# Optimization experiments

Measured on AMD Instinct MI355X. Metric: run time of the kernel, lower is better.

## Reference

```python
import jax, jax.numpy as jnp
import numpy as np

L, H, E, D, FF, V, CTX = 8, 16, 1024, 64, 4096, 2048, 2048
B, T = 4, 1024


def _ln(x, g, b, eps=1e-5):
    mu = x.mean(-1, keepdims=True)
    var = ((x - mu) ** 2).mean(-1, keepdims=True)
    return (x - mu) * jax.lax.rsqrt(var + eps) * g + b


def setup_inputs() -> dict:
    key = jax.random.key(0)
    ks = jax.random.split(key, 12)
    s = 0.02
    return {
        "tokens": jax.random.randint(ks[0], (B, T), 0, V),
        "tok_emb": jax.random.normal(ks[1], (V, E), jnp.float32) * s,
        "pos_emb": jax.random.normal(ks[2], (CTX, E), jnp.float32) * s,
        "Wq": jax.random.normal(ks[3], (L, H, E, D), jnp.float32) * s,
        "Wk": jax.random.normal(ks[4], (L, H, E, D), jnp.float32) * s,
        "Wv": jax.random.normal(ks[5], (L, H, E, D), jnp.float32) * s,
        "Wo": jax.random.normal(ks[6], (L, H * D, E), jnp.float32) * s,
        "bo": jnp.zeros((L, E), jnp.float32),
        "ln1_g": jnp.ones((L, E), jnp.float32),
        "ln1_b": jnp.zeros((L, E), jnp.float32),
        "ln2_g": jnp.ones((L, E), jnp.float32),
        "ln2_b": jnp.zeros((L, E), jnp.float32),
        "W1": jax.random.normal(ks[7], (L, E, FF), jnp.float32) * s,
        "b1": jnp.zeros((L, FF), jnp.float32),
        "W2": jax.random.normal(ks[8], (L, FF, E), jnp.float32) * s,
        "b2": jnp.zeros((L, E), jnp.float32),
        "lnf_g": jnp.ones((E,), jnp.float32),
        "lnf_b": jnp.zeros((E,), jnp.float32),
        "Wlm": jax.random.normal(ks[9], (E, V), jnp.float32) * s,
        "blm": jnp.zeros((V,), jnp.float32),
    }


def reference(tokens, tok_emb, pos_emb, Wq, Wk, Wv, Wo, bo, ln1_g, ln1_b,
              ln2_g, ln2_b, W1, b1, W2, b2, lnf_g, lnf_b, Wlm, blm):
    # NOTE: original indexes pos_embd with token ids (pos_embd(x.int()))
    x = tok_emb[tokens] + pos_emb[tokens]  # [B,T,E]
    t = x.shape[1]
    causal = jnp.tril(jnp.ones((t, t), bool))
    scale = 1.0 / jnp.sqrt(jnp.float32(D))
    for l in range(L):
        x = _ln(x, ln1_g[l], ln1_b[l])
        q = jnp.einsum('bte,hed->bhtd', x, Wq[l])
        k = jnp.einsum('bte,hed->bhtd', x, Wk[l])
        v = jnp.einsum('bte,hed->bhtd', x, Wv[l])
        scores = jnp.einsum('bhtd,bhsd->bhts', q, k) * scale
        scores = jnp.where(causal, scores, -jnp.inf)
        att = jax.nn.softmax(scores, axis=-1)
        o = jnp.einsum('bhts,bhsd->bhtd', att, v)
        o = o.transpose(0, 2, 1, 3).reshape(x.shape[0], t, H * D)
        x = x + o @ Wo[l] + bo[l]
        x = _ln(x, ln2_g[l], ln2_b[l])
        x = x + jax.nn.relu(x @ W1[l] + b1[l]) @ W2[l] + b2[l]
    x = _ln(x, lnf_g, lnf_b)
    return x @ Wlm + blm
```

## Files before the change

kernel.cpp:

```cpp
#include <hip/hip_runtime.h>
#include <hip/hip_bf16.h>

#define LAYERS 8
#define H_ 16
#define E_ 1024
#define D_ 64
#define FF_ 4096
#define V_ 2048
#define B_ 4
#define T_ 1024
#define MTOK (B_*T_)

typedef __bf16 bf16x8_t __attribute__((ext_vector_type(8)));
typedef __bf16 bf16x4_t __attribute__((ext_vector_type(4)));
typedef float f32x4_t __attribute__((ext_vector_type(4)));
typedef __hip_bfloat16 bf16_t;

__device__ __forceinline__ bf16_t f2b(float f) { return __float2bfloat16(f); }

__global__ void embed_kernel(const int* __restrict__ tokens,
                             const float* __restrict__ te,
                             const float* __restrict__ pe,
                             bf16_t* __restrict__ x) {
  int row = blockIdx.x;
  int tok = tokens[row];
  int t = threadIdx.x;
  float4 va = ((const float4*)(te + (size_t)tok * E_))[t];
  float4 vp = ((const float4*)(pe + (size_t)tok * E_))[t];
  bf16x4_t o;
  o[0] = (__bf16)(va.x + vp.x); o[1] = (__bf16)(va.y + vp.y);
  o[2] = (__bf16)(va.z + vp.z); o[3] = (__bf16)(va.w + vp.w);
  ((bf16x4_t*)(x + (size_t)row * E_))[t] = o;
}

__global__ __launch_bounds__(256) void ln_kernel(const bf16_t* __restrict__ xin,
                                                 bf16_t* __restrict__ xout,
                                                 const float* __restrict__ g,
                                                 const float* __restrict__ b) {
  int row = blockIdx.x, tid = threadIdx.x;
  bf16x4_t v4 = ((const bf16x4_t*)(xin + (size_t)row * E_))[tid];
  float v0 = (float)v4[0], v1 = (float)v4[1], v2 = (float)v4[2], v3 = (float)v4[3];
  float s  = v0 + v1 + v2 + v3;
  float sq = v0*v0 + v1*v1 + v2*v2 + v3*v3;
  for (int off = 32; off; off >>= 1) {
    s  += __shfl_xor(s, off, 64);
    sq += __shfl_xor(sq, off, 64);
  }
  __shared__ float2 wred[4];
  if ((tid & 63) == 0) wred[tid >> 6] = make_float2(s, sq);
  __syncthreads();
  float2 w0 = wred[0], w1 = wred[1], w2 = wred[2], w3 = wred[3];
  float S = w0.x + w1.x + w2.x + w3.x, SQ = w0.y + w1.y + w2.y + w3.y;
  float mean = S * (1.0f / E_);
  float var  = SQ * (1.0f / E_) - mean * mean;
  float inv = rsqrtf(var + 1e-5f);
  float4 gv = ((const float4*)g)[tid];
  float4 bv = ((const float4*)b)[tid];
  bf16x4_t o;
  o[0] = (__bf16)((v0 - mean) * inv * gv.x + bv.x);
  o[1] = (__bf16)((v1 - mean) * inv * gv.y + bv.y);
  o[2] = (__bf16)((v2 - mean) * inv * gv.z + bv.z);
  o[3] = (__bf16)((v3 - mean) * inv * gv.w + bv.w);
  ((bf16x4_t*)(xout + (size_t)row * E_))[tid] = o;
}

__global__ __launch_bounds__(256) void reduce_ln_kernel(
    const bf16_t* __restrict__ p,
    const bf16_t* __restrict__ tin,
    const float* __restrict__ bias,
    bf16_t* __restrict__ r,
    bf16_t* __restrict__ tout,
    const float* __restrict__ g,
    const float* __restrict__ b) {
  int row = blockIdx.x, tid = threadIdx.x;
  size_t base = (size_t)row * E_ + tid * 4;
  bf16x4_t tv = *(const bf16x4_t*)(tin + base);
  bf16x4_t p0 = *(const bf16x4_t*)(p + base);
  bf16x4_t p1 = *(const bf16x4_t*)(p + (size_t)MTOK * E_ + base);
  float4 bv = ((const float4*)bias)[tid];
  float y0 = (float)tv[0] + (float)p0[0] + (float)p1[0] + bv.x;
  float y1 = (float)tv[1] + (float)p0[1] + (float)p1[1] + bv.y;
  float y2 = (float)tv[2] + (float)p0[2] + (float)p1[2] + bv.z;
  float y3 = (float)tv[3] + (float)p0[3] + (float)p1[3] + bv.w;
  bf16x4_t rv;
  rv[0] = (__bf16)y0; rv[1] = (__bf16)y1; rv[2] = (__bf16)y2; rv[3] = (__bf16)y3;
  *(bf16x4_t*)(r + base) = rv;
  float z0 = (float)rv[0], z1 = (float)rv[1], z2 = (float)rv[2], z3 = (float)rv[3];
  float s = z0 + z1 + z2 + z3, sq = z0*z0 + z1*z1 + z2*z2 + z3*z3;
  for (int off = 32; off; off >>= 1) {
    s  += __shfl_xor(s, off, 64);
    sq += __shfl_xor(sq, off, 64);
  }
  __shared__ float2 wred[4];
  if ((tid & 63) == 0) wred[tid >> 6] = make_float2(s, sq);
  __syncthreads();
  float2 w0 = wred[0], w1 = wred[1], w2 = wred[2], w3 = wred[3];
  float S = w0.x + w1.x + w2.x + w3.x, SQ = w0.y + w1.y + w2.y + w3.y;
  float mean = S * (1.0f / E_);
  float var  = SQ * (1.0f / E_) - mean * mean;
  float inv = rsqrtf(var + 1e-5f);
  float4 gv = ((const float4*)g)[tid];
  float4 b2v = ((const float4*)b)[tid];
  bf16x4_t o;
  o[0] = (__bf16)((z0 - mean) * inv * gv.x + b2v.x);
  o[1] = (__bf16)((z1 - mean) * inv * gv.y + b2v.y);
  o[2] = (__bf16)((z2 - mean) * inv * gv.z + b2v.z);
  o[3] = (__bf16)((z3 - mean) * inv * gv.w + b2v.w);
  *(bf16x4_t*)(tout + base) = o;
}

__global__ void prep_weights_kernel(const float* __restrict__ Wq,
                                    const float* __restrict__ Wk,
                                    const float* __restrict__ Wv,
                                    const float* __restrict__ Wo,
                                    const float* __restrict__ W1,
                                    const float* __restrict__ W2,
                                    bf16_t* __restrict__ WqkvT,
                                    bf16_t* __restrict__ WoT,
                                    bf16_t* __restrict__ W1T,
                                    bf16_t* __restrict__ W2T,
                                    int l) {
  __shared__ float tile[32][33];
  int bid = blockIdx.x;
  const float* src; bf16_t* dst; int R, C, r0, c0;
  if (bid < 3072) {
    int op = bid >> 10, rem = bid & 1023;
    int h = rem >> 6, tt = rem & 63;
    const float* W = (op == 0) ? Wq : (op == 1) ? Wk : Wv;
    src = W + (size_t)l * H_ * E_ * D_ + (size_t)h * E_ * D_;
    dst = WqkvT + (size_t)op * E_ * H_ * D_ + (size_t)h * E_ * D_;
    R = E_; C = D_; r0 = (tt >> 1) * 32; c0 = (tt & 1) * 32;
  } else if (bid < 4096) {
    int tt = bid - 3072;
    src = Wo + (size_t)l * H_ * D_ * E_; dst = WoT;
    R = H_ * D_; C = E_; r0 = (tt >> 5) * 32; c0 = (tt & 31) * 32;
  } else if (bid < 8192) {
    int tt = bid - 4096;
    src = W1 + (size_t)l * E_ * FF_; dst = W1T;
    R = E_; C = FF_; r0 = (tt >> 7) * 32; c0 = (tt & 127) * 32;
  } else {
    int tt = bid - 8192;
    src = W2 + (size_t)l * FF_ * E_; dst = W2T;
    R = FF_; C = E_; r0 = (tt >> 5) * 32; c0 = (tt & 31) * 32;
  }
  int tx = threadIdx.x, ty = threadIdx.y;
  for (int i = 0; i < 4; i++)
    tile[ty + i * 8][tx] = src[(size_t)(r0 + ty + i * 8) * C + (c0 + tx)];
  __syncthreads();
  for (int i = 0; i < 4; i++)
    dst[(size_t)(c0 + ty + i * 8) * R + (r0 + tx)] = f2b(tile[tx][ty + i * 8]);
}

__global__ void transpose_kernel(const float* __restrict__ in, bf16_t* __restrict__ out,
                                 int R, int C) {
  __shared__ float tile[32][33];
  int r0 = blockIdx.y * 32, c0 = blockIdx.x * 32;
  int tx = threadIdx.x, ty = threadIdx.y;
  for (int i = 0; i < 4; i++)
    tile[ty + i * 8][tx] = in[(size_t)(r0 + ty + i * 8) * C + (c0 + tx)];
  __syncthreads();
  for (int i = 0; i < 4; i++)
    out[(size_t)(c0 + ty + i * 8) * R + (r0 + tx)] = f2b(tile[tx][ty + i * 8]);
}

enum { MODE_F32 = 0, MODE_BF16 = 1, MODE_QKV = 2, MODE_BF16R = 3 };

__device__ __forceinline__ void gload16(const bf16_t* g, bf16_t* l) {
  __builtin_amdgcn_global_load_lds((const __attribute__((address_space(1))) void*)g,
                                   (__attribute__((address_space(3))) void*)l, 16, 0, 0);
}

__device__ __forceinline__ int xcd_swz(int flat, int nwg) {
  int q = nwg >> 3, r = nwg & 7;
  int xcd = flat & 7, idx = flat >> 3;
  return (xcd < r ? xcd * (q + 1) : r * (q + 1) + (xcd - r) * q) + idx;
}

#define BK 32
template <int BM, int BN, int MODE>
__global__ __launch_bounds__(256) void gemm97_kernel(
    const bf16_t* __restrict__ A, long long sAz, int lda,
    const bf16_t* __restrict__ Bt, long long sBz, int ldb,
    void* __restrict__ C, long long sCz,
    const float* __restrict__ bias,
    const void* __restrict__ resid,
    int M, int N, int K, int relu) {
  constexpr int FR = BM / 32, FC = BN / 32;
  constexpr int A_ISS = BM / 64, B_ISS = BN / 64;
  __shared__ __align__(16) bf16_t As[2][BM * BK];
  __shared__ __align__(16) bf16_t Bs[2][BN * BK];
  int tid = threadIdx.x;
  int z = blockIdx.z;
  int nwg = gridDim.x * gridDim.y;
  int flat = xcd_swz(blockIdx.y * gridDim.x + blockIdx.x, nwg);
  int m0 = (flat / gridDim.x) * BM, n0 = (flat % gridDim.x) * BN;
  const bf16_t* Ab = A + (size_t)z * sAz + (size_t)m0 * lda;
  const bf16_t* Bb = Bt + (size_t)z * sBz + (size_t)n0 * ldb;
  int lane = tid & 63, wave = tid >> 6;
  int wr = (wave >> 1) * (BM / 2), wc = (wave & 1) * (BN / 2);
  int lr = lane & 15, lk = (lane >> 4) * 8;
  int srow = tid >> 2;
  int scol = (tid & 3) * 8;

  f32x4_t acc[FR][FC];
  for (int i = 0; i < FR; i++)
    for (int j = 0; j < FC; j++)
      acc[i][j] = (f32x4_t){0.f, 0.f, 0.f, 0.f};

  auto stage = [&](int buf, int k0) {
#pragma unroll
    for (int i = 0; i < A_ISS; i++)
      gload16(Ab + (size_t)(i * 64 + srow) * lda + k0 + scol, &As[buf][i * 2048 + wave * 512]);
#pragma unroll
    for (int i = 0; i < B_ISS; i++)
      gload16(Bb + (size_t)(i * 64 + srow) * ldb + k0 + scol, &Bs[buf][i * 2048 + wave * 512]);
  };

  int nk = K / BK;
  stage(0, 0);
  __syncthreads();
  int cur = 0;
  for (int kt = 0; kt < nk; ++kt) {
    if (kt + 1 < nk) stage(cur ^ 1, (kt + 1) * BK);
    bf16x8_t af[FR], bfv[FC];
#pragma unroll
    for (int i = 0; i < FR; i++)
      af[i] = *(const bf16x8_t*)(&As[cur][(wr + i * 16 + lr) * BK + lk]);
#pragma unroll
    for (int j = 0; j < FC; j++)
      bfv[j] = *(const bf16x8_t*)(&Bs[cur][(wc + j * 16 + lr) * BK + lk]);
#pragma unroll
    for (int i = 0; i < FR; i++)
#pragma unroll
      for (int j = 0; j < FC; j++)
        acc[i][j] = __builtin_amdgcn_mfma_f32_16x16x32_bf16(af[i], bfv[j], acc[i][j], 0, 0, 0);
    __syncthreads();
    cur ^= 1;
  }

#pragma unroll
  for (int i = 0; i < FR; i++)
#pragma unroll
    for (int j = 0; j < FC; j++) {
      f32x4_t v = acc[i][j];
      int n = n0 + wc + j * 16 + lr;
      int mb = m0 + wr + i * 16 + (lane >> 4) * 4;
#pragma unroll
      for (int r = 0; r < 4; r++) {
        int m = mb + r;
        float val = v[r];
        if (bias) val += bias[n];
        if (relu) val = fmaxf(val, 0.f);
        if (MODE == MODE_F32) {
          size_t idx = (size_t)z * sCz + (size_t)m * N + n;
          ((float*)C)[idx] = val;
        } else if (MODE == MODE_BF16) {
          size_t idx = (size_t)z * sCz + (size_t)m * N + n;
          ((bf16_t*)C)[idx] = f2b(val);
        } else if (MODE == MODE_BF16R) {
          size_t idx = (size_t)m * N + n;
          val += __bfloat162float(((const bf16_t*)resid)[idx]);
          ((bf16_t*)C)[idx] = f2b(val);
        } else {
          int sect = n >> 10, hd = n & 1023, h = hd >> 6, d = hd & 63;
          int b = m >> 10, t = m & 1023;
          size_t base = (size_t)sect * ((size_t)B_ * H_ * T_ * D_);
          size_t idx = base + ((size_t)(b * H_ + h) << 16) +
                       (sect == 2 ? (size_t)((d << 10) + t) : (size_t)((t << 6) + d));
          ((bf16_t*)C)[idx] = f2b(val);
        }
      }
    }
}

template <int MODE>
__global__ __launch_bounds__(512) void gemm3_kernel(
    const bf16_t* __restrict__ A, int lda,
    const bf16_t* __restrict__ Bt, int ldb,
    void* __restrict__ C, long long sCz,
    const float* __restrict__ bias,
    int M, int N, int kspan, int relu) {
  constexpr int ABUFE = 256 * 64;
  constexpr int BBUFE = 128 * 64;
  __shared__ __align__(16) bf16_t LA[3 * ABUFE];
  __shared__ __align__(16) bf16_t LB[3 * BBUFE];
  int tid = threadIdx.x, lane = tid & 63, wave = tid >> 6;
  int wm = wave >> 1, wn = wave & 1;
  int z = blockIdx.z;
  int nwg = gridDim.x * gridDim.y;
  int flat = xcd_swz(blockIdx.y * gridDim.x + blockIdx.x, nwg);
  int m0 = (flat / gridDim.x) * 256, n0 = (flat % gridDim.x) * 128;
  const bf16_t* Ab = A + (size_t)m0 * lda + (size_t)z * kspan;
  const bf16_t* Bb = Bt + (size_t)n0 * ldb + (size_t)z * kspan;
  int sr = lane & 15, sc = (lane >> 4) * 8;

  f32x4_t acc[4][4];
#pragma unroll
  for (int i = 0; i < 4; i++)
#pragma unroll
    for (int j = 0; j < 4; j++)
      acc[i][j] = (f32x4_t){0.f, 0.f, 0.f, 0.f};

  auto stageh = [&](int b, int kt, int h) {
    int kg = kt * 64;
#pragma unroll
    for (int ch = 0; ch < 2; ch++) {
      int sub = wave * 4 + 2 * h + ch;
      gload16(Ab + (size_t)((sub >> 1) * 16 + sr) * lda + kg + (sub & 1) * 32 + sc,
              LA + b * ABUFE + sub * 512);
    }
    {
      int sub = wave * 2 + h;
      gload16(Bb + (size_t)((sub >> 1) * 16 + sr) * ldb + kg + (sub & 1) * 32 + sc,
              LB + b * BBUFE + sub * 512);
    }
  };

  auto phase = [&](int b, int ks, int t, int nk) {
    bf16x8_t af[4], bfv[4];
    unsigned abase = (unsigned)(size_t)(LA + b * ABUFE);
    unsigned bbase = (unsigned)(size_t)(LB + b * BBUFE);
#pragma unroll
    for (int i = 0; i < 4; i++) {
      unsigned ad = abase + (unsigned)((((wm * 4 + i) * 2 + ks) * 512 + lane * 8) * 2);
      asm volatile("ds_read_b128 %0, %1" : "=v"(af[i]) : "v"(ad));
    }
#pragma unroll
    for (int j = 0; j < 4; j++) {
      unsigned bd = bbase + (unsigned)((((wn * 4 + j) * 2 + ks) * 512 + lane * 8) * 2);
      asm volatile("ds_read_b128 %0, %1" : "=v"(bfv[j]) : "v"(bd));
    }
    if (t + 2 < nk) stageh((t + 2) % 3, t + 2, ks);
    __builtin_amdgcn_s_barrier();
    asm volatile("s_waitcnt lgkmcnt(0)" ::: "memory");
    __builtin_amdgcn_sched_barrier(0);
    __builtin_amdgcn_s_setprio(1);
#pragma unroll
    for (int i = 0; i < 4; i++)
#pragma unroll
      for (int j = 0; j < 4; j++)
        acc[i][j] = __builtin_amdgcn_mfma_f32_16x16x32_bf16(af[i], bfv[j], acc[i][j], 0, 0, 0);
    __builtin_amdgcn_s_setprio(0);
  };

  int nk = kspan / 64;
  stageh(0, 0, 0); stageh(0, 0, 1);
  stageh(1, 1, 0); stageh(1, 1, 1);
  for (int t = 0; t < nk; ++t) {
    int b = t % 3;
    if (t + 1 < nk) { asm volatile("s_waitcnt vmcnt(6)" ::: "memory"); }
    else            { asm volatile("s_waitcnt vmcnt(0)" ::: "memory"); }
    __builtin_amdgcn_s_barrier();
    phase(b, 0, t, nk);
    phase(b, 1, t, nk);
  }

#pragma unroll
  for (int i = 0; i < 4; i++)
#pragma unroll
    for (int j = 0; j < 4; j++) {
      f32x4_t v = acc[i][j];
      int n = n0 + wn * 64 + j * 16 + (lane & 15);
      int mb = m0 + wm * 64 + i * 16 + (lane >> 4) * 4;
#pragma unroll
      for (int r = 0; r < 4; r++) {
        int m = mb + r;
        float val = v[r];
        if (bias) val += bias[n];
        if (relu) val = fmaxf(val, 0.f);
        if (MODE == MODE_F32) {
          size_t idx = (size_t)z * sCz + (size_t)m * N + n;
          ((float*)C)[idx] = val;
        } else {
          size_t idx = (size_t)z * sCz + (size_t)m * N + n;
          ((bf16_t*)C)[idx] = f2b(val);
        }
      }
    }
}

#define KPAD 72

__global__ __launch_bounds__(256) void flash_kernel(
    const bf16_t* __restrict__ q,
    const bf16_t* __restrict__ kk,
    const bf16_t* __restrict__ vt,
    bf16_t* __restrict__ o) {
  __shared__ __align__(16) bf16_t Ks[64 * KPAD];
  __shared__ __align__(16) bf16_t Vs[64 * KPAD];
  __shared__ __align__(16) bf16_t Ps[4][16 * KPAD];
  int bid = blockIdx.x;
  int qi = 15 - (bid >> 6);
  int bh = bid & 63;
  int b = bh >> 4, h = bh & 15;
  const bf16_t* qb = q + ((size_t)bh << 16);
  const bf16_t* kb = kk + ((size_t)bh << 16);
  const bf16_t* vb = vt + ((size_t)bh << 16);
  int tid = threadIdx.x, lane = tid & 63, wave = tid >> 6;
  int lr = lane & 15, lg = lane >> 4;
  int qbase = qi * 64;

  bf16x8_t qf[2];
  {
    const bf16_t* qrow = qb + (size_t)(qbase + wave * 16 + lr) * D_ + lg * 8;
    qf[0] = *(const bf16x8_t*)(qrow);
    qf[1] = *(const bf16x8_t*)(qrow + 32);
  }

  float m_r[4], l_r[4];
  f32x4_t oc[4];
#pragma unroll
  for (int r = 0; r < 4; r++) { m_r[r] = -1e30f; l_r[r] = 0.f; }
#pragma unroll
  for (int j = 0; j < 4; j++) oc[j] = (f32x4_t){0.f, 0.f, 0.f, 0.f};

  int srow = tid >> 2, scol = (tid & 3) * 16;

  bf16x8_t k0, k1, v0, v1;
  {
    const bf16_t* kg = kb + (size_t)srow * D_ + scol;
    k0 = *(const bf16x8_t*)kg;
    k1 = *(const bf16x8_t*)(kg + 8);
    const bf16_t* vg = vb + (size_t)srow * T_ + scol;
    v0 = *(const bf16x8_t*)vg;
    v1 = *(const bf16x8_t*)(vg + 8);
  }

  for (int s = 0; s <= qi; s++) {
    __syncthreads();
    *(bf16x8_t*)(&Ks[srow * KPAD + scol]) = k0;
    *(bf16x8_t*)(&Ks[srow * KPAD + scol + 8]) = k1;
    *(bf16x8_t*)(&Vs[srow * KPAD + scol]) = v0;
    *(bf16x8_t*)(&Vs[srow * KPAD + scol + 8]) = v1;
    __syncthreads();

    if (s < qi) {
      int kv1 = (s + 1) * 64;
      const bf16_t* kg = kb + (size_t)(kv1 + srow) * D_ + scol;
      k0 = *(const bf16x8_t*)kg;
      k1 = *(const bf16x8_t*)(kg + 8);
      const bf16_t* vg = vb + (size_t)srow * T_ + kv1 + scol;
      v0 = *(const bf16x8_t*)vg;
      v1 = *(const bf16x8_t*)(vg + 8);
    }

    int kv0 = s * 64;
    f32x4_t sc[4];
#pragma unroll
    for (int j = 0; j < 4; j++) {
      f32x4_t a = (f32x4_t){0.f, 0.f, 0.f, 0.f};
      bf16x8_t b0 = *(const bf16x8_t*)(&Ks[(j * 16 + lr) * KPAD + lg * 8]);
      bf16x8_t b1 = *(const bf16x8_t*)(&Ks[(j * 16 + lr) * KPAD + lg * 8 + 32]);
      a = __builtin_amdgcn_mfma_f32_16x16x32_bf16(qf[0], b0, a, 0, 0, 0);
      a = __builtin_amdgcn_mfma_f32_16x16x32_bf16(qf[1], b1, a, 0, 0, 0);
      sc[j] = a;
    }
    if (s == qi) {
#pragma unroll
      for (int j = 0; j < 4; j++)
#pragma unroll
        for (int r = 0; r < 4; r++) {
          int kvp = kv0 + j * 16 + lr;
          int qp  = qbase + wave * 16 + lg * 4 + r;
          sc[j][r] = (kvp <= qp) ? sc[j][r] * 0.125f : -1e30f;
        }
    } else {
#pragma unroll
      for (int j = 0; j < 4; j++)
#pragma unroll
        for (int r = 0; r < 4; r++) sc[j][r] *= 0.125f;
    }

    float pm[4];
#pragma unroll
    for (int r = 0; r < 4; r++) {
      float v = fmaxf(fmaxf(sc[0][r], sc[1][r]), fmaxf(sc[2][r], sc[3][r]));
      v = fmaxf(v, __shfl_xor(v, 1, 64));
      v = fmaxf(v, __shfl_xor(v, 2, 64));
      v = fmaxf(v, __shfl_xor(v, 4, 64));
      v = fmaxf(v, __shfl_xor(v, 8, 64));
      pm[r] = v;
    }
    bool ok = (pm[0] - m_r[0] <= 8.f) && (pm[1] - m_r[1] <= 8.f) &&
              (pm[2] - m_r[2] <= 8.f) && (pm[3] - m_r[3] <= 8.f);
    if (!__all(ok)) {
#pragma unroll
      for (int r = 0; r < 4; r++) {
        float mn = fmaxf(m_r[r], pm[r]);
        float ex = __expf(m_r[r] - mn);
        m_r[r] = mn;
        l_r[r] *= ex;
#pragma unroll
        for (int j = 0; j < 4; j++) oc[j][r] *= ex;
      }
    }
#pragma unroll
    for (int j = 0; j < 4; j++)
#pragma unroll
      for (int r = 0; r < 4; r++) {
        float p = __expf(sc[j][r] - m_r[r]);
        l_r[r] += p;
        Ps[wave][(lg * 4 + r) * KPAD + j * 16 + lr] = f2b(p);
      }

    bf16x8_t pa0 = *(const bf16x8_t*)(&Ps[wave][lr * KPAD + lg * 8]);
    bf16x8_t pa1 = *(const bf16x8_t*)(&Ps[wave][lr * KPAD + lg * 8 + 32]);
#pragma unroll
    for (int j = 0; j < 4; j++) {
      bf16x8_t vb0 = *(const bf16x8_t*)(&Vs[(j * 16 + lr) * KPAD + lg * 8]);
      bf16x8_t vb1 = *(const bf16x8_t*)(&Vs[(j * 16 + lr) * KPAD + lg * 8 + 32]);
      oc[j] = __builtin_amdgcn_mfma_f32_16x16x32_bf16(pa0, vb0, oc[j], 0, 0, 0);
      oc[j] = __builtin_amdgcn_mfma_f32_16x16x32_bf16(pa1, vb1, oc[j], 0, 0, 0);
    }
  }

#pragma unroll
  for (int r = 0; r < 4; r++) {
    float v = l_r[r];
    v += __shfl_xor(v, 1, 64);
    v += __shfl_xor(v, 2, 64);
    v += __shfl_xor(v, 4, 64);
    v += __shfl_xor(v, 8, 64);
    l_r[r] = 1.f / v;
  }
  bf16_t* ob = o + ((size_t)(b * T_ + qbase + wave * 16)) * (H_ * D_) + h * D_;
#pragma unroll
  for (int j = 0; j < 4; j++)
#pragma unroll
    for (int r = 0; r < 4; r++) {
      int qrow = lg * 4 + r;
      ob[(size_t)qrow * (H_ * D_) + j * 16 + lr] = f2b(oc[j][r] * l_r[r]);
    }
}

extern "C" void kernel_launch(void* const* d_in, const int* in_sizes, int n_in,
                              void* d_out, int out_size, void* d_ws, size_t ws_size,
                              hipStream_t stream) {
  (void)in_sizes; (void)n_in; (void)out_size; (void)ws_size;
  const int*   tokens = (const int*)d_in[0];
  const float* tok_emb = (const float*)d_in[1];
  const float* pos_emb = (const float*)d_in[2];
  const float* Wq = (const float*)d_in[3];
  const float* Wk = (const float*)d_in[4];
  const float* Wv = (const float*)d_in[5];
  const float* Wo = (const float*)d_in[6];
  const float* bo = (const float*)d_in[7];
  const float* ln1_g = (const float*)d_in[8];
  const float* ln1_b = (const float*)d_in[9];
  const float* ln2_g = (const float*)d_in[10];
  const float* ln2_b = (const float*)d_in[11];
  const float* W1 = (const float*)d_in[12];
  const float* b1 = (const float*)d_in[13];
  const float* W2 = (const float*)d_in[14];
  const float* b2 = (const float*)d_in[15];
  const float* lnf_g = (const float*)d_in[16];
  const float* lnf_b = (const float*)d_in[17];
  const float* Wlm = (const float*)d_in[18];
  const float* blm = (const float*)d_in[19];

  char* w = (char*)d_ws;
  size_t off = 0;
  auto alloc = [&](size_t bytes) { void* p = (void*)(w + off); off += (bytes + 255) & ~(size_t)255; return p; };
  bf16_t* r    = (bf16_t*)alloc((size_t)MTOK * E_ * 2);
  bf16_t* t    = (bf16_t*)alloc((size_t)MTOK * E_ * 2);
  bf16_t* q    = (bf16_t*)alloc((size_t)B_ * H_ * T_ * D_ * 2);
  bf16_t* kk   = (bf16_t*)alloc((size_t)B_ * H_ * T_ * D_ * 2);
  bf16_t* vt   = (bf16_t*)alloc((size_t)B_ * H_ * T_ * D_ * 2);
  bf16_t* o    = (bf16_t*)alloc((size_t)MTOK * E_ * 2);
  bf16_t* h1   = (bf16_t*)alloc((size_t)MTOK * FF_ * 2);
  bf16_t* WqkvT = (bf16_t*)alloc((size_t)3 * E_ * H_ * D_ * 2);
  bf16_t* WoT  = (bf16_t*)alloc((size_t)E_ * H_ * D_ * 2);
  bf16_t* W1T  = (bf16_t*)alloc((size_t)E_ * FF_ * 2);
  bf16_t* W2T  = (bf16_t*)alloc((size_t)E_ * FF_ * 2);
  bf16_t* WlmT = (bf16_t*)alloc((size_t)E_ * V_ * 2);
  bf16_t* p2   = (bf16_t*)alloc((size_t)2 * MTOK * E_ * 2);

  embed_kernel<<<MTOK, 256, 0, stream>>>(tokens, tok_emb, pos_emb, r);
  transpose_kernel<<<dim3(V_ / 32, E_ / 32), dim3(32, 8), 0, stream>>>(Wlm, WlmT, E_, V_);
  ln_kernel<<<MTOK, 256, 0, stream>>>(r, t, ln1_g, ln1_b);

  for (int l = 0; l < LAYERS; l++) {
    prep_weights_kernel<<<12288, dim3(32, 8), 0, stream>>>(
        Wq, Wk, Wv, Wo, W1, W2, WqkvT, WoT, W1T, W2T, l);

    gemm97_kernel<128, 128, MODE_QKV><<<dim3(24, 32, 1), 256, 0, stream>>>(
        t, 0, E_, WqkvT, 0, E_, q, 0, nullptr, nullptr, MTOK, 3 * H_ * D_, E_, 0);

    flash_kernel<<<1024, 256, 0, stream>>>(q, kk, vt, o);

    gemm97_kernel<128, 128, MODE_BF16R><<<dim3(8, 32, 1), 256, 0, stream>>>(
        o, 0, H_ * D_, WoT, 0, H_ * D_, r, 0, bo + l * E_, t, MTOK, E_, H_ * D_, 0);

    ln_kernel<<<MTOK, 256, 0, stream>>>(r, t, ln2_g + l * E_, ln2_b + l * E_);

    gemm3_kernel<MODE_BF16><<<dim3(32, 16, 1), 512, 0, stream>>>(
        t, E_, W1T, E_, h1, 0, b1 + l * FF_, MTOK, FF_, E_, 1);
    gemm3_kernel<MODE_BF16><<<dim3(8, 16, 2), 512, 0, stream>>>(
        h1, FF_, W2T, FF_, p2, (long long)MTOK * E_, nullptr, MTOK, E_, FF_ / 2, 0);
    const float* gn = (l + 1 < LAYERS) ? (ln1_g + (l + 1) * E_) : lnf_g;
    const float* bn = (l + 1 < LAYERS) ? (ln1_b + (l + 1) * E_) : lnf_b;
    reduce_ln_kernel<<<MTOK, 256, 0, stream>>>(p2, t, b2 + l * E_, r, t, gn, bn);
  }

  gemm3_kernel<MODE_F32><<<dim3(16, 16, 1), 512, 0, stream>>>(
      t, E_, WlmT, E_, d_out, 0, blm, MTOK, V_, E_, 0);
}
```

Baseline: 2.098 ms.

## Vectorize LN kernels to two rows per block, widen weight transpose tiles, add MFMA priority

The LayerNorm and residual+LayerNorm kernels now process two rows per 256-thread block, with 8-element bf16 vector loads and stores per thread. The per-layer weight prep transpose moves from 32x32 to 64x64 tiles, using float4 reads and 16-byte bf16 writes to cut launch count and raise memory-transaction width. The flash attention kernel wraps its MFMA blocks in s_setprio to favour matrix issue over other waves. The changes aim to reduce memory-bound overhead in the small kernels; the transpose now does strided LDS column reads that may cause bank conflicts.

```diff
diff --git a/kernel.cpp b/kernel.cpp
--- a/kernel.cpp
+++ b/kernel.cpp
@@ -37,11 +37,15 @@
                                                  bf16_t* __restrict__ xout,
                                                  const float* __restrict__ g,
                                                  const float* __restrict__ b) {
-  int row = blockIdx.x, tid = threadIdx.x;
-  bf16x4_t v4 = ((const bf16x4_t*)(xin + (size_t)row * E_))[tid];
-  float v0 = (float)v4[0], v1 = (float)v4[1], v2 = (float)v4[2], v3 = (float)v4[3];
-  float s  = v0 + v1 + v2 + v3;
-  float sq = v0*v0 + v1*v1 + v2*v2 + v3*v3;
+  int tid = threadIdx.x;
+  int row = blockIdx.x * 2 + (tid >> 7);
+  int li = tid & 127;
+  size_t base = (size_t)row * E_ + li * 8;
+  bf16x8_t v8 = *(const bf16x8_t*)(xin + base);
+  float z[8];
+  float s = 0.f, sq = 0.f;
+#pragma unroll
+  for (int j = 0; j < 8; j++) { z[j] = (float)v8[j]; s += z[j]; sq += z[j] * z[j]; }
   for (int off = 32; off; off >>= 1) {
     s  += __shfl_xor(s, off, 64);
     sq += __shfl_xor(sq, off, 64);
@@ -49,19 +53,19 @@
   __shared__ float2 wred[4];
   if ((tid & 63) == 0) wred[tid >> 6] = make_float2(s, sq);
   __syncthreads();
-  float2 w0 = wred[0], w1 = wred[1], w2 = wred[2], w3 = wred[3];
-  float S = w0.x + w1.x + w2.x + w3.x, SQ = w0.y + w1.y + w2.y + w3.y;
+  int wb = (tid >> 7) << 1;
+  float S = wred[wb].x + wred[wb + 1].x, SQ = wred[wb].y + wred[wb + 1].y;
   float mean = S * (1.0f / E_);
   float var  = SQ * (1.0f / E_) - mean * mean;
   float inv = rsqrtf(var + 1e-5f);
-  float4 gv = ((const float4*)g)[tid];
-  float4 bv = ((const float4*)b)[tid];
-  bf16x4_t o;
-  o[0] = (__bf16)((v0 - mean) * inv * gv.x + bv.x);
-  o[1] = (__bf16)((v1 - mean) * inv * gv.y + bv.y);
-  o[2] = (__bf16)((v2 - mean) * inv * gv.z + bv.z);
-  o[3] = (__bf16)((v3 - mean) * inv * gv.w + bv.w);
-  ((bf16x4_t*)(xout + (size_t)row * E_))[tid] = o;
+  float4 g0 = *(const float4*)(g + li * 8), g1 = *(const float4*)(g + li * 8 + 4);
+  float4 b0 = *(const float4*)(b + li * 8), b1 = *(const float4*)(b + li * 8 + 4);
+  float gg[8] = {g0.x, g0.y, g0.z, g0.w, g1.x, g1.y, g1.z, g1.w};
+  float bb[8] = {b0.x, b0.y, b0.z, b0.w, b1.x, b1.y, b1.z, b1.w};
+  bf16x8_t o;
+#pragma unroll
+  for (int j = 0; j < 8; j++) o[j] = (__bf16)((z[j] - mean) * inv * gg[j] + bb[j]);
+  *(bf16x8_t*)(xout + base) = o;
 }
 
 __global__ __launch_bounds__(256) void reduce_ln_kernel(
@@ -72,21 +76,26 @@
     bf16_t* __restrict__ tout,
     const float* __restrict__ g,
     const float* __restrict__ b) {
-  int row = blockIdx.x, tid = threadIdx.x;
-  size_t base = (size_t)row * E_ + tid * 4;
-  bf16x4_t tv = *(const bf16x4_t*)(tin + base);
-  bf16x4_t p0 = *(const bf16x4_t*)(p + base);
-  bf16x4_t p1 = *(const bf16x4_t*)(p + (size_t)MTOK * E_ + base);
-  float4 bv = ((const float4*)bias)[tid];
-  float y0 = (float)tv[0] + (float)p0[0] + (float)p1[0] + bv.x;
-  float y1 = (float)tv[1] + (float)p0[1] + (float)p1[1] + bv.y;
-  float y2 = (float)tv[2] + (float)p0[2] + (float)p1[2] + bv.z;
-  float y3 = (float)tv[3] + (float)p0[3] + (float)p1[3] + bv.w;
-  bf16x4_t rv;
-  rv[0] = (__bf16)y0; rv[1] = (__bf16)y1; rv[2] = (__bf16)y2; rv[3] = (__bf16)y3;
-  *(bf16x4_t*)(r + base) = rv;
-  float z0 = (float)rv[0], z1 = (float)rv[1], z2 = (float)rv[2], z3 = (float)rv[3];
-  float s = z0 + z1 + z2 + z3, sq = z0*z0 + z1*z1 + z2*z2 + z3*z3;
+  int tid = threadIdx.x;
+  int row = blockIdx.x * 2 + (tid >> 7);
+  int li = tid & 127;
+  size_t base = (size_t)row * E_ + li * 8;
+  bf16x8_t tv = *(const bf16x8_t*)(tin + base);
+  bf16x8_t p0 = *(const bf16x8_t*)(p + base);
+  bf16x8_t p1 = *(const bf16x8_t*)(p + (size_t)MTOK * E_ + base);
+  float4 c0 = *(const float4*)(bias + li * 8), c1 = *(const float4*)(bias + li * 8 + 4);
+  float bb[8] = {c0.x, c0.y, c0.z, c0.w, c1.x, c1.y, c1.z, c1.w};
+  bf16x8_t rv;
+  float z[8];
+  float s = 0.f, sq = 0.f;
+#pragma unroll
+  for (int j = 0; j < 8; j++) {
+    float y = (float)tv[j] + (float)p0[j] + (float)p1[j] + bb[j];
+    rv[j] = (__bf16)y;
+    z[j] = (float)rv[j];
+    s += z[j]; sq += z[j] * z[j];
+  }
+  *(bf16x8_t*)(r + base) = rv;
   for (int off = 32; off; off >>= 1) {
     s  += __shfl_xor(s, off, 64);
     sq += __shfl_xor(sq, off, 64);
@@ -94,61 +103,68 @@
   __shared__ float2 wred[4];
   if ((tid & 63) == 0) wred[tid >> 6] = make_float2(s, sq);
   __syncthreads();
-  float2 w0 = wred[0], w1 = wred[1], w2 = wred[2], w3 = wred[3];
-  float S = w0.x + w1.x + w2.x + w3.x, SQ = w0.y + w1.y + w2.y + w3.y;
+  int wb = (tid >> 7) << 1;
+  float S = wred[wb].x + wred[wb + 1].x, SQ = wred[wb].y + wred[wb + 1].y;
   float mean = S * (1.0f / E_);
   float var  = SQ * (1.0f / E_) - mean * mean;
   float inv = rsqrtf(var + 1e-5f);
-  float4 gv = ((const float4*)g)[tid];
-  float4 b2v = ((const float4*)b)[tid];
-  bf16x4_t o;
-  o[0] = (__bf16)((z0 - mean) * inv * gv.x + b2v.x);
-  o[1] = (__bf16)((z1 - mean) * inv * gv.y + b2v.y);
-  o[2] = (__bf16)((z2 - mean) * inv * gv.z + b2v.z);
-  o[3] = (__bf16)((z3 - mean) * inv * gv.w + b2v.w);
-  *(bf16x4_t*)(tout + base) = o;
-}
-
-__global__ void prep_weights_kernel(const float* __restrict__ Wq,
-                                    const float* __restrict__ Wk,
-                                    const float* __restrict__ Wv,
-                                    const float* __restrict__ Wo,
-                                    const float* __restrict__ W1,
-                                    const float* __restrict__ W2,
-                                    bf16_t* __restrict__ WqkvT,
-                                    bf16_t* __restrict__ WoT,
-                                    bf16_t* __restrict__ W1T,
-                                    bf16_t* __restrict__ W2T,
-                                    int l) {
-  __shared__ float tile[32][33];
-  int bid = blockIdx.x;
+  float4 g0 = *(const float4*)(g + li * 8), g1 = *(const float4*)(g + li * 8 + 4);
+  float4 d0 = *(const float4*)(b + li * 8), d1 = *(const float4*)(b + li * 8 + 4);
+  float gg[8] = {g0.x, g0.y, g0.z, g0.w, g1.x, g1.y, g1.z, g1.w};
+  float dd[8] = {d0.x, d0.y, d0.z, d0.w, d1.x, d1.y, d1.z, d1.w};
+  bf16x8_t o;
+#pragma unroll
+  for (int j = 0; j < 8; j++) o[j] = (__bf16)((z[j] - mean) * inv * gg[j] + dd[j]);
+  *(bf16x8_t*)(tout + base) = o;
+}
+
+__global__ __launch_bounds__(256) void prep_weights_kernel(
+    const float* __restrict__ Wq, const float* __restrict__ Wk,
+    const float* __restrict__ Wv, const float* __restrict__ Wo,
+    const float* __restrict__ W1, const float* __restrict__ W2,
+    bf16_t* __restrict__ WqkvT, bf16_t* __restrict__ WoT,
+    bf16_t* __restrict__ W1T, bf16_t* __restrict__ W2T, int l) {
+  __shared__ float tile[64][65];
+  int bid = blockIdx.x, tid = threadIdx.x;
   const float* src; bf16_t* dst; int R, C, r0, c0;
-  if (bid < 3072) {
-    int op = bid >> 10, rem = bid & 1023;
-    int h = rem >> 6, tt = rem & 63;
+  if (bid < 768) {
+    int op = bid >> 8, rem = bid & 255;
+    int h = rem >> 4, tt = rem & 15;
     const float* W = (op == 0) ? Wq : (op == 1) ? Wk : Wv;
     src = W + (size_t)l * H_ * E_ * D_ + (size_t)h * E_ * D_;
     dst = WqkvT + (size_t)op * E_ * H_ * D_ + (size_t)h * E_ * D_;
-    R = E_; C = D_; r0 = (tt >> 1) * 32; c0 = (tt & 1) * 32;
-  } else if (bid < 4096) {
-    int tt = bid - 3072;
+    R = E_; C = D_; r0 = tt * 64; c0 = 0;
+  } else if (bid < 1024) {
+    int tt = bid - 768;
     src = Wo + (size_t)l * H_ * D_ * E_; dst = WoT;
-    R = H_ * D_; C = E_; r0 = (tt >> 5) * 32; c0 = (tt & 31) * 32;
-  } else if (bid < 8192) {
-    int tt = bid - 4096;
+    R = H_ * D_; C = E_; r0 = (tt >> 4) * 64; c0 = (tt & 15) * 64;
+  } else if (bid < 2048) {
+    int tt = bid - 1024;
     src = W1 + (size_t)l * E_ * FF_; dst = W1T;
-    R = E_; C = FF_; r0 = (tt >> 7) * 32; c0 = (tt & 127) * 32;
+    R = E_; C = FF_; r0 = (tt >> 6) * 64; c0 = (tt & 63) * 64;
   } else {
-    int tt = bid - 8192;
+    int tt = bid - 2048;
     src = W2 + (size_t)l * FF_ * E_; dst = W2T;
-    R = FF_; C = E_; r0 = (tt >> 5) * 32; c0 = (tt & 31) * 32;
-  }
-  int tx = threadIdx.x, ty = threadIdx.y;
-  for (int i = 0; i < 4; i++)
-    tile[ty + i * 8][tx] = src[(size_t)(r0 + ty + i * 8) * C + (c0 + tx)];
+    R = FF_; C = E_; r0 = (tt >> 4) * 64; c0 = (tt & 15) * 64;
+  }
+#pragma unroll
+  for (int i = 0; i < 4; i++) {
+    int idx = i * 256 + tid;
+    int row = idx >> 4, q4 = (idx & 15) * 4;
+    float4 v = *(const float4*)(src + (size_t)(r0 + row) * C + c0 + q4);
+    tile[row][q4 + 0] = v.x; tile[row][q4 + 1] = v.y;
+    tile[row][q4 + 2] = v.z; tile[row][q4 + 3] = v.w;
+  }
   __syncthreads();
-  for (int i = 0; i < 4; i++)
-    dst[(size_t)(c0 + ty + i * 8) * R + (r0 + tx)] = f2b(tile[tx][ty + i * 8]);
+#pragma unroll
+  for (int i = 0; i < 2; i++) {
+    int idx = i * 256 + tid;
+    int c = idx >> 3, r8 = (idx & 7) * 8;
+    bf16x8_t ov;
+#pragma unroll
+    for (int j = 0; j < 8; j++) ov[j] = (__bf16)tile[r8 + j][c];
+    *(bf16x8_t*)(dst + (size_t)(c0 + c) * R + r0 + r8) = ov;
+  }
 }
 
 __global__ void transpose_kernel(const float* __restrict__ in, bf16_t* __restrict__ out,
@@ -446,6 +462,7 @@
 
     int kv0 = s * 64;
     f32x4_t sc[4];
+    __builtin_amdgcn_s_setprio(1);
 #pragma unroll
     for (int j = 0; j < 4; j++) {
       f32x4_t a = (f32x4_t){0.f, 0.f, 0.f, 0.f};
@@ -455,6 +472,7 @@
       a = __builtin_amdgcn_mfma_f32_16x16x32_bf16(qf[1], b1, a, 0, 0, 0);
       sc[j] = a;
     }
+    __builtin_amdgcn_s_setprio(0);
     if (s == qi) {
 #pragma unroll
       for (int j = 0; j < 4; j++)
@@ -505,6 +523,7 @@
 
     bf16x8_t pa0 = *(const bf16x8_t*)(&Ps[wave][lr * KPAD + lg * 8]);
     bf16x8_t pa1 = *(const bf16x8_t*)(&Ps[wave][lr * KPAD + lg * 8 + 32]);
+    __builtin_amdgcn_s_setprio(1);
 #pragma unroll
     for (int j = 0; j < 4; j++) {
       bf16x8_t vb0 = *(const bf16x8_t*)(&Vs[(j * 16 + lr) * KPAD + lg * 8]);
@@ -512,6 +531,7 @@
       oc[j] = __builtin_amdgcn_mfma_f32_16x16x32_bf16(pa0, vb0, oc[j], 0, 0, 0);
       oc[j] = __builtin_amdgcn_mfma_f32_16x16x32_bf16(pa1, vb1, oc[j], 0, 0, 0);
     }
+    __builtin_amdgcn_s_setprio(0);
   }
 
 #pragma unroll
@@ -577,10 +597,10 @@
 
   embed_kernel<<<MTOK, 256, 0, stream>>>(tokens, tok_emb, pos_emb, r);
   transpose_kernel<<<dim3(V_ / 32, E_ / 32), dim3(32, 8), 0, stream>>>(Wlm, WlmT, E_, V_);
-  ln_kernel<<<MTOK, 256, 0, stream>>>(r, t, ln1_g, ln1_b);
+  ln_kernel<<<MTOK / 2, 256, 0, stream>>>(r, t, ln1_g, ln1_b);
 
   for (int l = 0; l < LAYERS; l++) {
-    prep_weights_kernel<<<12288, dim3(32, 8), 0, stream>>>(
+    prep_weights_kernel<<<3072, 256, 0, stream>>>(
         Wq, Wk, Wv, Wo, W1, W2, WqkvT, WoT, W1T, W2T, l);
 
     gemm97_kernel<128, 128, MODE_QKV><<<dim3(24, 32, 1), 256, 0, stream>>>(
@@ -591,7 +611,7 @@
     gemm97_kernel<128, 128, MODE_BF16R><<<dim3(8, 32, 1), 256, 0, stream>>>(
         o, 0, H_ * D_, WoT, 0, H_ * D_, r, 0, bo + l * E_, t, MTOK, E_, H_ * D_, 0);
 
-    ln_kernel<<<MTOK, 256, 0, stream>>>(r, t, ln2_g + l * E_, ln2_b + l * E_);
+    ln_kernel<<<MTOK / 2, 256, 0, stream>>>(r, t, ln2_g + l * E_, ln2_b + l * E_);
 
     gemm3_kernel<MODE_BF16><<<dim3(32, 16, 1), 512, 0, stream>>>(
         t, E_, W1T, E_, h1, 0, b1 + l * FF_, MTOK, FF_, E_, 1);
@@ -599,7 +619,7 @@
         h1, FF_, W2T, FF_, p2, (long long)MTOK * E_, nullptr, MTOK, E_, FF_ / 2, 0);
     const float* gn = (l + 1 < LAYERS) ? (ln1_g + (l + 1) * E_) : lnf_g;
     const float* bn = (l + 1 < LAYERS) ? (ln1_b + (l + 1) * E_) : lnf_b;
-    reduce_ln_kernel<<<MTOK, 256, 0, stream>>>(p2, t, b2 + l * E_, r, t, gn, bn);
+    reduce_ln_kernel<<<MTOK / 2, 256, 0, stream>>>(p2, t, b2 + l * E_, r, t, gn, bn);
   }
 
   gemm3_kernel<MODE_F32><<<dim3(16, 16, 1), 512, 0, stream>>>(
```

Measured after the change: 2.076 ms. About the same (-1.0%).
